# Optimization experiments

Hardware: AMD Instinct MI355X
Metric: run time of the kernel (lower is better)

## Reference

```python
import jax, jax.numpy as jnp
import numpy as np

B, N, F_IN, H, C, K = 32, 1024, 128, 64, 32, 2
L_HOP, NUM_ITER, TEMP = 2, 5, 0.5


def setup_inputs() -> dict:
    key = jax.random.key(0)
    ks = jax.random.split(key, 8)
    x = jax.random.normal(ks[0], (B, N, F_IN), jnp.float32)
    adj = jax.random.randint(ks[1], (B, N, N), 0, 2, jnp.int32)  # dense 0/1 adjacency per graph
    W_gcn = jax.random.normal(ks[2], (F_IN, H), jnp.float32) / np.sqrt(F_IN)
    b_gcn = jnp.zeros((H,), jnp.float32)
    W_unary = jax.random.normal(ks[3], (H, C), jnp.float32) / np.sqrt(H)
    b_unary = jnp.zeros((C,), jnp.float32)
    means = jax.random.normal(ks[4], (K, H), jnp.float32)
    scales = jnp.ones((K, H), jnp.float32) * 8.0  # widened so exp(-dist) stays in fp32 range
    kw = jnp.ones((K,), jnp.float32)
    mu = jax.random.normal(ks[5], (C, C), jnp.float32)
    return dict(x=x, adj=adj, W_gcn=W_gcn, b_gcn=b_gcn, W_unary=W_unary,
                b_unary=b_unary, means=means, scales=scales, kw=kw, mu=mu)


def _forward(x, adj_f, W_gcn, b_gcn, W_unary, b_unary, means, scales, kw, mu):
    n = x.shape[1]
    # --- GCN encode: D^{-1/2}(A+I)D^{-1/2} X W + b, relu ---
    a_hat = adj_f + jnp.eye(n, dtype=adj_f.dtype)
    dinv = jax.lax.rsqrt(a_hat.sum(-1))                       # [B,N], deg >= 1 via self-loop
    norm = dinv[:, :, None] * a_hat * dinv[:, None, :]        # [B,N,N]
    h = jax.nn.relu(jnp.einsum('bij,bjf,fh->bih', norm, x, W_gcn) + b_gcn)  # [B,N,H]
    # --- l-hop reachability mask ---
    adj_l = adj_f
    for _ in range(L_HOP - 1):
        adj_l = adj_l @ adj_f
    adj_l = (adj_l > 0).astype(h.dtype)                       # [B,N,N]
    # --- unary potentials ---
    unary = h @ W_unary + b_unary                             # [B,N,C]
    # --- Gaussian kernel: w_k * exp(dist_i[k] + dist_j[k]) == (e*w) @ e.T ---
    diff = (h[:, :, None, :] - means) / scales                # [B,N,K,H]
    e = jnp.exp(-jnp.sum(diff * diff, -1))                    # [B,N,K]
    pairwise = jnp.einsum('bik,k,bjk->bij', e, kw, e) * adj_l  # [B,N,N]
    # --- mean-field CRF iterations ---
    Q = jax.nn.softmax(unary, -1)
    for _ in range(NUM_ITER):
        msg = jnp.einsum('bij,bjc->bic', pairwise, Q @ mu)
        Q = jax.nn.softmax((unary + msg) / TEMP, -1)
    # --- soft-cluster pooling ---
    x_pooled = jnp.einsum('bnc,bnh->bch', Q, h)               # [B,C,H]
    adj_pooled = jnp.einsum('bnc,bnm,bmd->bcd', Q, adj_f, Q)  # [B,C,C]
    return x_pooled, adj_pooled


def reference(x, adj, W_gcn, b_gcn, W_unary, b_unary, means, scales, kw, mu):
    return _forward(x, adj.astype(x.dtype), W_gcn, b_gcn, W_unary, b_unary,
                    means, scales, kw, mu)
```

## Files before the change

### kernel.cpp

```cpp
#include <hip/hip_runtime.h>
#include <stdint.h>

#define NB  32
#define NN  1024
#define FIN 128
#define HH  64
#define CC  32
#define ZCAP 16
#define NITER 5

using short8  = __attribute__((ext_vector_type(8))) short;
using floatx4 = __attribute__((ext_vector_type(4))) float;

__device__ inline float b2f(unsigned short u) {
  union { uint32_t i; float f; } v; v.i = ((uint32_t)u) << 16; return v.f;
}
__device__ inline float b2f_lo(uint32_t w) {
  union { uint32_t i; float f; } v; v.i = w << 16; return v.f;
}
__device__ inline float b2f_hi(uint32_t w) {
  union { uint32_t i; float f; } v; v.i = w & 0xFFFF0000u; return v.f;
}
__device__ inline unsigned short f2b(float f) {
  union { uint32_t i; float f; } v; v.f = f;
  uint32_t r = v.i + 0x7FFFu + ((v.i >> 16) & 1u);
  return (unsigned short)(r >> 16);
}
__device__ inline floatx4 zf4() { floatx4 v = {0.f, 0.f, 0.f, 0.f}; return v; }

__global__ __launch_bounds__(256) void k_wcvt(const float* __restrict__ Wg,
    const float* __restrict__ Wu, unsigned short* __restrict__ Wgt,
    unsigned short* __restrict__ Wut, float* __restrict__ out, int out_n) {
  const int t = threadIdx.x;
  for (int idx = t; idx < HH * FIN; idx += 256) {
    int hh = idx >> 7, f = idx & 127;
    Wgt[idx] = f2b(Wg[f * HH + hh]);
  }
  for (int idx = t; idx < CC * HH; idx += 256) {
    int c = idx >> 6, f = idx & 63;
    Wut[idx] = f2b(Wu[f * CC + c]);
  }
  for (int idx = t; idx < out_n; idx += 256) out[idx] = 0.f;
}

__global__ __launch_bounds__(256) void k_bits(const int* __restrict__ adj,
    uint32_t* __restrict__ rowbits, float* __restrict__ dinv,
    int* __restrict__ zcnt) {
  __shared__ uint32_t rw[4][32];
  const int t = threadIdx.x, g = t >> 6, lane = t & 63;
  if (lane < 32) rw[g][lane] = 0u;
  __syncthreads();
  const size_t row = (size_t)blockIdx.x * 4 + g;
  int s = 0;
  #pragma unroll
  for (int rep = 0; rep < 4; rep++) {
    int4 a = ((const int4*)(adj + row * NN))[rep * 64 + lane];
    int b0 = (a.x != 0), b1 = (a.y != 0), b2 = (a.z != 0), b3 = (a.w != 0);
    uint32_t nib = ((uint32_t)(b0 | (b1 << 1) | (b2 << 2) | (b3 << 3))) << ((lane & 7) * 4);
    atomicOr(&rw[g][rep * 8 + (lane >> 3)], nib);
    s += b0 + b1 + b2 + b3;
  }
  #pragma unroll
  for (int m = 1; m < 64; m <<= 1) s += __shfl_xor(s, m, 64);
  __syncthreads();
  if (lane < 32) rowbits[row * 32 + lane] = rw[g][lane];
  if (lane == 0) { dinv[row] = rsqrtf((float)s + 1.0f); zcnt[row] = 0; }
}

__global__ __launch_bounds__(256) void k_cbits(const uint32_t* __restrict__ rowbits,
    uint32_t* __restrict__ colbits) {
  __shared__ uint32_t rbL[512 * 32];
  const int bid = blockIdx.x;
  const int b = bid >> 3, half = (bid >> 2) & 1, jt = bid & 3;
  const int t = threadIdx.x;
  const uint32_t* src = rowbits + ((size_t)b * NN + half * 512) * 32;
  for (int idx = t; idx < 512 * 32; idx += 256) rbL[idx] = src[idx];
  __syncthreads();
  const int j = jt * 256 + t, jw = j >> 5, jb = j & 31;
  uint32_t out[16];
  for (int w = 0; w < 16; w++) {
    uint32_t acc = 0;
    #pragma unroll
    for (int r = 0; r < 32; r++)
      acc |= ((rbL[(w * 32 + r) * 32 + jw] >> jb) & 1u) << r;
    out[w] = acc;
  }
  uint4* dst = (uint4*)(colbits + ((size_t)b * NN + j) * 32 + half * 16);
  #pragma unroll
  for (int x = 0; x < 4; x++) {
    uint4 v; v.x = out[4*x]; v.y = out[4*x+1]; v.z = out[4*x+2]; v.w = out[4*x+3];
    dst[x] = v;
  }
}

__global__ __launch_bounds__(256) void k_xw(const float* __restrict__ x,
    const unsigned short* __restrict__ Wgt, const float* __restrict__ dinv,
    unsigned short* __restrict__ xs, unsigned short* __restrict__ xst) {
  const int bid = blockIdx.x;
  const int b = bid >> 4;
  const int m0 = (bid & 15) * 64;
  const int t = threadIdx.x, wv = t >> 6, lane = t & 63, l15 = lane & 15, q = lane >> 4;
  const int mb = m0 + wv * 16;
  floatx4 acc[4];
  #pragma unroll
  for (int u = 0; u < 4; u++) acc[u] = zf4();
  #pragma unroll
  for (int k0 = 0; k0 < FIN; k0 += 32) {
    const float4* xp = (const float4*)(x + ((size_t)b * NN + mb + l15) * FIN + k0 + q * 8);
    float4 a0 = xp[0], a1 = xp[1];
    short8 af;
    af[0] = (short)f2b(a0.x); af[1] = (short)f2b(a0.y);
    af[2] = (short)f2b(a0.z); af[3] = (short)f2b(a0.w);
    af[4] = (short)f2b(a1.x); af[5] = (short)f2b(a1.y);
    af[6] = (short)f2b(a1.z); af[7] = (short)f2b(a1.w);
    #pragma unroll
    for (int u = 0; u < 4; u++) {
      short8 bf = *(const short8*)(Wgt + (u * 16 + l15) * FIN + k0 + q * 8);
      acc[u] = __builtin_amdgcn_mfma_f32_16x16x32_bf16(af, bf, acc[u], 0, 0, 0);
    }
  }
  #pragma unroll
  for (int r = 0; r < 4; r++) {
    const int i = mb + q * 4 + r;
    const float dv = dinv[b * NN + i];
    #pragma unroll
    for (int u = 0; u < 4; u++) {
      const int c = u * 16 + l15;
      unsigned short bv = f2b(dv * acc[u][r]);
      xs[((size_t)b * NN + i) * HH + c] = bv;
      xst[((size_t)b * HH + c) * NN + i] = bv;
    }
  }
}

__global__ __launch_bounds__(256) void k_gcnun(const uint32_t* __restrict__ rowbits,
    const unsigned short* __restrict__ xst, const unsigned short* __restrict__ xs,
    const float* __restrict__ dinv, const float* __restrict__ bg,
    const float* __restrict__ means, const float* __restrict__ scales,
    const unsigned short* __restrict__ Wut, const float* __restrict__ bu,
    float* __restrict__ h, float* __restrict__ e2, float* __restrict__ unary) {
  __shared__ unsigned short hsh[4][16][72];
  const int bid = blockIdx.x;
  const int b = bid >> 4;
  const int m0 = (bid & 15) * 64;
  const int t = threadIdx.x, wv = t >> 6, lane = t & 63, l15 = lane & 15, q = lane >> 4;
  const int mb = m0 + wv * 16;
  floatx4 acc[4];
  #pragma unroll
  for (int u = 0; u < 4; u++) acc[u] = zf4();
  const uint32_t* rbrow = rowbits + ((size_t)b * NN + mb + l15) * 32;
  for (int k0 = 0; k0 < NN; k0 += 32) {
    uint32_t sh = rbrow[k0 >> 5] >> (q * 8);
    short8 af;
    #pragma unroll
    for (int jj = 0; jj < 8; jj++)
      af[jj] = (short)(((sh >> jj) & 1u) ? 0x3F80 : 0);
    #pragma unroll
    for (int u = 0; u < 4; u++) {
      short8 bf = *(const short8*)(xst + ((size_t)b * HH + u * 16 + l15) * NN + k0 + q * 8);
      acc[u] = __builtin_amdgcn_mfma_f32_16x16x32_bf16(af, bf, acc[u], 0, 0, 0);
    }
  }
  float bgc[4], mn0[4], mn1[4], is0[4], is1[4];
  #pragma unroll
  for (int u = 0; u < 4; u++) {
    const int c = u * 16 + l15;
    bgc[u] = bg[c];
    mn0[u] = means[c];        is0[u] = 1.0f / scales[c];
    mn1[u] = means[HH + c];   is1[u] = 1.0f / scales[HH + c];
  }
  #pragma unroll
  for (int r = 0; r < 4; r++) {
    const int i = mb + q * 4 + r;
    const float dv = dinv[b * NN + i];
    float dd0 = 0.f, dd1 = 0.f;
    #pragma unroll
    for (int u = 0; u < 4; u++) {
      const int c = u * 16 + l15;
      float xsv = b2f(xs[((size_t)b * NN + i) * HH + c]);
      float v = dv * (acc[u][r] + xsv) + bgc[u];
      v = v > 0.f ? v : 0.f;
      h[((size_t)b * NN + i) * HH + c] = v;
      unsigned short hb = f2b(v);
      hsh[wv][q * 4 + r][c] = hb;
      float vb = b2f(hb);
      float t0 = (vb - mn0[u]) * is0[u]; dd0 += t0 * t0;
      float t1 = (vb - mn1[u]) * is1[u]; dd1 += t1 * t1;
    }
    #pragma unroll
    for (int m = 1; m < 16; m <<= 1) {
      dd0 += __shfl_xor(dd0, m, 64);
      dd1 += __shfl_xor(dd1, m, 64);
    }
    if (l15 == 0) {
      e2[((size_t)b * NN + i) * 2 + 0] = __expf(-dd0);
      e2[((size_t)b * NN + i) * 2 + 1] = __expf(-dd1);
    }
  }
  floatx4 uacc[2];
  uacc[0] = zf4(); uacc[1] = zf4();
  #pragma unroll
  for (int k0 = 0; k0 < HH; k0 += 32) {
    short8 af = *(const short8*)&hsh[wv][l15][k0 + q * 8];
    #pragma unroll
    for (int u = 0; u < 2; u++) {
      short8 bf = *(const short8*)(Wut + (u * 16 + l15) * HH + k0 + q * 8);
      uacc[u] = __builtin_amdgcn_mfma_f32_16x16x32_bf16(af, bf, uacc[u], 0, 0, 0);
    }
  }
  const float bu0 = bu[l15], bu1 = bu[16 + l15];
  #pragma unroll
  for (int r = 0; r < 4; r++) {
    const int i = mb + q * 4 + r;
    unary[((size_t)b * NN + i) * CC + l15] = uacc[0][r] + bu0;
    unary[((size_t)b * NN + i) * CC + 16 + l15] = uacc[1][r] + bu1;
  }
}

__global__ __launch_bounds__(256) void k_zscan(const uint32_t* __restrict__ rowbits,
    const uint32_t* __restrict__ colbits, int* __restrict__ zcnt,
    int* __restrict__ zidx) {
  __shared__ uint32_t rwL[128 * 32];
  const int bid = blockIdx.x;
  const int b = bid >> 3, it = bid & 7;
  const int i0 = it * 128;
  const int t = threadIdx.x;
  #pragma unroll
  for (int x = 0; x < 16; x++)
    rwL[x * 256 + t] = rowbits[((size_t)b * NN + i0) * 32 + x * 256 + t];
  __syncthreads();
  for (int jc = 0; jc < 4; jc++) {
    const int j = jc * 256 + t;
    uint32_t cb[32];
    const uint4* cbp = (const uint4*)(colbits + ((size_t)b * NN + j) * 32);
    #pragma unroll
    for (int x = 0; x < 8; x++) {
      uint4 v = cbp[x];
      cb[4*x] = v.x; cb[4*x+1] = v.y; cb[4*x+2] = v.z; cb[4*x+3] = v.w;
    }
    for (int i = 0; i < 128; i++) {
      uint32_t m = 0;
      for (int w = 0; w < 32; w++) {
        m |= rwL[i * 32 + w] & cb[w];
        if (__all(m != 0)) break;
      }
      if (m == 0) {
        int old = atomicAdd(&zcnt[b * NN + i0 + i], 1);
        if (old < ZCAP) zidx[(size_t)(b * NN + i0 + i) * ZCAP + old] = j;
      }
    }
  }
}

__global__ __launch_bounds__(256) void k_crf1(const float* __restrict__ unary,
    const float* __restrict__ e2g, const float* __restrict__ kwp,
    const float* __restrict__ mu, const uint32_t* __restrict__ rowbits,
    const uint32_t* __restrict__ colbits, const int* __restrict__ zcnt,
    const int* __restrict__ zidx, const float* __restrict__ h,
    unsigned short* __restrict__ qtb, float* __restrict__ out) {
  __shared__ uint32_t QLu[NN * 17];
  __shared__ float eL[NN * 2];
  __shared__ float muL[CC * CC];
  __shared__ float part[4][64];
  __shared__ float Tf[64];
  __shared__ float S[64];
  const int bid = blockIdx.x;
  const int b = bid >> 2, seg = bid & 3;
  const int t = threadIdx.x;
  const float kw0 = kwp[0], kw1 = kwp[1];
  for (int i = t; i < CC * CC; i += 256) muL[i] = mu[i];
  for (int n = t; n < NN; n += 256) {
    float2 ev = ((const float2*)(e2g + ((size_t)b * NN + n) * 2))[0];
    eL[n * 2] = ev.x; eL[n * 2 + 1] = ev.y;
    float lg[CC];
    const float4* ur = (const float4*)(unary + ((size_t)b * NN + n) * CC);
    #pragma unroll
    for (int c4 = 0; c4 < 8; c4++) {
      float4 v = ur[c4];
      lg[c4*4] = v.x; lg[c4*4+1] = v.y; lg[c4*4+2] = v.z; lg[c4*4+3] = v.w;
    }
    float mx = lg[0];
    #pragma unroll
    for (int c = 1; c < CC; c++) mx = fmaxf(mx, lg[c]);
    float s = 0.f;
    #pragma unroll
    for (int c = 0; c < CC; c++) { lg[c] = __expf(lg[c] - mx); s += lg[c]; }
    float inv = 1.f / s;
    #pragma unroll
    for (int d2 = 0; d2 < 16; d2++)
      QLu[n * 17 + d2] = (uint32_t)f2b(lg[2*d2] * inv)
                       | ((uint32_t)f2b(lg[2*d2+1] * inv) << 16);
  }
  __syncthreads();
  const int kd = t & 63, dd = t & 31, kk = (t >> 5) & 1, sub = t >> 6;
  for (int it = 0; it < NITER; it++) {
    float s = 0.f;
    for (int jj = 0; jj < 256; jj++) {
      const int j = sub * 256 + jj;
      const float ej = eL[j * 2 + kk];
      const uint32_t w = QLu[j * 17 + (dd >> 1)];
      s += ej * ((dd & 1) ? b2f_hi(w) : b2f_lo(w));
    }
    part[sub][kd] = s;
    __syncthreads();
    if (t < 64) Tf[t] = part[0][t] + part[1][t] + part[2][t] + part[3][t];
    __syncthreads();
    if (t < 64) {
      const int k = t >> 5, c = t & 31;
      float ss = 0.f;
      #pragma unroll 8
      for (int d = 0; d < CC; d++) ss += Tf[k * 32 + d] * muL[d * 32 + c];
      S[t] = ((k == 0) ? kw0 : kw1) * ss;
    }
    __syncthreads();
    uint32_t newq[4][16];
    #pragma unroll
    for (int rep = 0; rep < 4; rep++) {
      const int n = rep * 256 + t;
      const float e0 = eL[n * 2], e1 = eL[n * 2 + 1];
      float lg[CC];
      {
        const float4* ur = (const float4*)(unary + ((size_t)b * NN + n) * CC);
        const float4* S0 = (const float4*)S;
        const float4* S1 = (const float4*)(S + 32);
        #pragma unroll
        for (int c4 = 0; c4 < 8; c4++) {
          float4 uv = ur[c4], s0 = S0[c4], s1 = S1[c4];
          lg[c4*4]   = uv.x + e0 * s0.x + e1 * s1.x;
          lg[c4*4+1] = uv.y + e0 * s0.y + e1 * s1.y;
          lg[c4*4+2] = uv.z + e0 * s0.z + e1 * s1.z;
          lg[c4*4+3] = uv.w + e0 * s0.w + e1 * s1.w;
        }
      }
      const int zc = zcnt[b * NN + n];
      if (zc > 0) {
        if (zc <= ZCAP) {
          for (int z = 0; z < zc; z++) {
            const int j = zidx[(size_t)(b * NN + n) * ZCAP + z];
            const float w = kw0 * e0 * eL[j * 2] + kw1 * e1 * eL[j * 2 + 1];
            for (int d2 = 0; d2 < 16; d2++) {
              const uint32_t wq = QLu[j * 17 + d2];
              const float w0 = w * b2f_lo(wq), w1 = w * b2f_hi(wq);
              #pragma unroll 8
              for (int c = 0; c < CC; c++)
                lg[c] -= w0 * muL[(2*d2) * 32 + c] + w1 * muL[(2*d2+1) * 32 + c];
            }
          }
        } else {
          const uint32_t* rbi = rowbits + ((size_t)b * NN + n) * 32;
          for (int j = 0; j < NN; j++) {
            uint32_t m = 0;
            const uint32_t* cbj = colbits + ((size_t)b * NN + j) * 32;
            for (int w32 = 0; w32 < 32; w32++) m |= rbi[w32] & cbj[w32];
            if (m == 0) {
              const float w = kw0 * e0 * eL[j * 2] + kw1 * e1 * eL[j * 2 + 1];
              for (int d2 = 0; d2 < 16; d2++) {
                const uint32_t wq = QLu[j * 17 + d2];
                const float w0 = w * b2f_lo(wq), w1 = w * b2f_hi(wq);
                #pragma unroll 8
                for (int c = 0; c < CC; c++)
                  lg[c] -= w0 * muL[(2*d2) * 32 + c] + w1 * muL[(2*d2+1) * 32 + c];
              }
            }
          }
        }
      }
      float mx = lg[0];
      #pragma unroll
      for (int c = 1; c < CC; c++) mx = fmaxf(mx, lg[c]);
      float ss = 0.f;
      #pragma unroll
      for (int c = 0; c < CC; c++) { lg[c] = __expf((lg[c] - mx) * 2.0f); ss += lg[c]; }
      const float inv = 1.f / ss;
      #pragma unroll
      for (int d2 = 0; d2 < 16; d2++)
        newq[rep][d2] = (uint32_t)f2b(lg[2*d2] * inv)
                      | ((uint32_t)f2b(lg[2*d2+1] * inv) << 16);
    }
    __syncthreads();
    #pragma unroll
    for (int rep = 0; rep < 4; rep++) {
      const int n = rep * 256 + t;
      #pragma unroll
      for (int d2 = 0; d2 < 16; d2++) QLu[n * 17 + d2] = newq[rep][d2];
    }
    __syncthreads();
  }
  {
    const int n = seg * 256 + t;
    #pragma unroll
    for (int d2 = 0; d2 < 16; d2++) {
      const uint32_t w = QLu[n * 17 + d2];
      qtb[((size_t)b * CC + 2*d2) * NN + n]     = (unsigned short)(w & 0xFFFFu);
      qtb[((size_t)b * CC + 2*d2 + 1) * NN + n] = (unsigned short)(w >> 16);
    }
  }
  {
    const int hh = t & 63, cg = t >> 6;
    float acc[8] = {0, 0, 0, 0, 0, 0, 0, 0};
    const int j0 = seg * 256;
    for (int jj = 0; jj < 256; jj++) {
      const int j = j0 + jj;
      const float hv = h[((size_t)b * NN + j) * HH + hh];
      #pragma unroll
      for (int w = 0; w < 4; w++) {
        const uint32_t q2 = QLu[j * 17 + cg * 4 + w];
        acc[2*w]     += b2f_lo(q2) * hv;
        acc[2*w + 1] += b2f_hi(q2) * hv;
      }
    }
    #pragma unroll
    for (int k = 0; k < 8; k++)
      atomicAdd(&out[((size_t)b * CC + cg * 8 + k) * HH + hh], acc[k]);
  }
}

__global__ __launch_bounds__(256) void k_adjqp(const uint32_t* __restrict__ rowbits,
    const unsigned short* __restrict__ qtb, float* __restrict__ out) {
  __shared__ float adjL[64][33];
  __shared__ float qL[64][32];
  const int bid = blockIdx.x;
  const int b = bid >> 4;
  const int m0 = (bid & 15) * 64;
  const int t = threadIdx.x, wv = t >> 6, lane = t & 63, l15 = lane & 15, q = lane >> 4;
  const int mb = m0 + wv * 16;
  floatx4 acc[2];
  acc[0] = zf4(); acc[1] = zf4();
  const uint32_t* rbrow = rowbits + ((size_t)b * NN + mb + l15) * 32;
  for (int k0 = 0; k0 < NN; k0 += 32) {
    uint32_t sh = rbrow[k0 >> 5] >> (q * 8);
    short8 af;
    #pragma unroll
    for (int jj = 0; jj < 8; jj++)
      af[jj] = (short)(((sh >> jj) & 1u) ? 0x3F80 : 0);
    #pragma unroll
    for (int u = 0; u < 2; u++) {
      short8 bf = *(const short8*)(qtb + ((size_t)b * CC + u * 16 + l15) * NN + k0 + q * 8);
      acc[u] = __builtin_amdgcn_mfma_f32_16x16x32_bf16(af, bf, acc[u], 0, 0, 0);
    }
  }
  #pragma unroll
  for (int r = 0; r < 4; r++)
    #pragma unroll
    for (int u = 0; u < 2; u++)
      adjL[wv * 16 + q * 4 + r][u * 16 + l15] = acc[u][r];
  #pragma unroll
  for (int x = 0; x < 8; x++) {
    const int idx = x * 256 + t;
    const int i = idx & 63, c = idx >> 6;
    qL[i][c] = b2f(qtb[((size_t)b * CC + c) * NN + m0 + i]);
  }
  __syncthreads();
  const int d = t & 31, cg = t >> 5;
  float a2[4] = {0, 0, 0, 0};
  for (int i = 0; i < 64; i++) {
    const float av = adjL[i][d];
    #pragma unroll
    for (int k = 0; k < 4; k++) a2[k] += qL[i][cg * 4 + k] * av;
  }
  #pragma unroll
  for (int k = 0; k < 4; k++)
    atomicAdd(&out[(size_t)NB * CC * HH + ((size_t)b * CC + cg * 4 + k) * CC + d], a2[k]);
}

extern "C" void kernel_launch(void* const* d_in, const int* in_sizes, int n_in,
                              void* d_out, int out_size, void* d_ws, size_t ws_size,
                              hipStream_t stream) {
  (void)in_sizes; (void)n_in; (void)out_size;
  const float* x      = (const float*)d_in[0];
  const int*   adj    = (const int*)d_in[1];
  const float* Wg     = (const float*)d_in[2];
  const float* bg     = (const float*)d_in[3];
  const float* Wu     = (const float*)d_in[4];
  const float* bu     = (const float*)d_in[5];
  const float* means  = (const float*)d_in[6];
  const float* scales = (const float*)d_in[7];
  const float* kw     = (const float*)d_in[8];
  const float* mu     = (const float*)d_in[9];

  char* ws = (char*)d_ws;
  size_t off = 0;
  auto alloc = [&](size_t bytes) { char* p = ws + off; off += (bytes + 255) & ~(size_t)255; return p; };
  uint32_t*       rbits = (uint32_t*)alloc((size_t)NB * NN * 32 * 4);
  uint32_t*       cbits = (uint32_t*)alloc((size_t)NB * NN * 32 * 4);
  float*          dinv  = (float*)alloc((size_t)NB * NN * 4);
  unsigned short* Wgt   = (unsigned short*)alloc((size_t)HH * FIN * 2);
  unsigned short* Wut   = (unsigned short*)alloc((size_t)CC * HH * 2);
  unsigned short* xs    = (unsigned short*)alloc((size_t)NB * NN * HH * 2);
  unsigned short* xst   = (unsigned short*)alloc((size_t)NB * HH * NN * 2);
  float*          h     = (float*)alloc((size_t)NB * NN * HH * 4);
  float*          e2    = (float*)alloc((size_t)NB * NN * 2 * 4);
  float*          unary = (float*)alloc((size_t)NB * NN * CC * 4);
  int*            zcnt  = (int*)alloc((size_t)NB * NN * 4);
  int*            zidx  = (int*)alloc((size_t)NB * NN * ZCAP * 4);
  unsigned short* qtb   = (unsigned short*)alloc((size_t)NB * CC * NN * 2);
  if (off > ws_size) return;

  float* out = (float*)d_out;
  const int out_n = NB * CC * (HH + CC);

  k_wcvt <<<1, 256, 0, stream>>>(Wg, Wu, Wgt, Wut, out, out_n);
  k_bits <<<NB * NN / 4, 256, 0, stream>>>(adj, rbits, dinv, zcnt);
  k_cbits<<<NB * 8, 256, 0, stream>>>(rbits, cbits);
  k_zscan<<<NB * 8, 256, 0, stream>>>(rbits, cbits, zcnt, zidx);
  k_xw   <<<NB * 16, 256, 0, stream>>>(x, Wgt, dinv, xs, xst);
  k_gcnun<<<NB * 16, 256, 0, stream>>>(rbits, xst, xs, dinv, bg, means, scales,
                                       Wut, bu, h, e2, unary);
  k_crf1 <<<NB * 4, 256, 0, stream>>>(unary, e2, kw, mu, rbits, cbits,
                                      zcnt, zidx, h, qtb, out);
  k_adjqp<<<NB * 16, 256, 0, stream>>>(rbits, qtb, out);
}
```

Measured before the change: 437.8 us.

## Split CRF iterations into per-iteration kernels with global Q ping-pong

```diff
diff --git a/kernel.cpp b/kernel.cpp
--- a/kernel.cpp
+++ b/kernel.cpp
@@ -138,11 +138,14 @@
     const float* __restrict__ dinv, const float* __restrict__ bg,
     const float* __restrict__ means, const float* __restrict__ scales,
     const unsigned short* __restrict__ Wut, const float* __restrict__ bu,
-    float* __restrict__ h, float* __restrict__ e2, float* __restrict__ unary) {
+    float* __restrict__ h, float* __restrict__ e2, float* __restrict__ unary,
+    unsigned short* __restrict__ Q0, float* __restrict__ Tp0) {
   __shared__ unsigned short hsh[4][16][72];
+  __shared__ float Qs0[64][33];
+  __shared__ float es0[64][2];
   const int bid = blockIdx.x;
-  const int b = bid >> 4;
-  const int m0 = (bid & 15) * 64;
+  const int b = bid >> 4, blk = bid & 15;
+  const int m0 = blk * 64;
   const int t = threadIdx.x, wv = t >> 6, lane = t & 63, l15 = lane & 15, q = lane >> 4;
   const int mb = m0 + wv * 16;
   floatx4 acc[4];
@@ -193,8 +196,11 @@
       dd1 += __shfl_xor(dd1, m, 64);
     }
     if (l15 == 0) {
-      e2[((size_t)b * NN + i) * 2 + 0] = __expf(-dd0);
-      e2[((size_t)b * NN + i) * 2 + 1] = __expf(-dd1);
+      float ev0 = __expf(-dd0), ev1 = __expf(-dd1);
+      e2[((size_t)b * NN + i) * 2 + 0] = ev0;
+      e2[((size_t)b * NN + i) * 2 + 1] = ev1;
+      es0[wv * 16 + q * 4 + r][0] = ev0;
+      es0[wv * 16 + q * 4 + r][1] = ev1;
     }
   }
   floatx4 uacc[2];
@@ -212,8 +218,32 @@
   #pragma unroll
   for (int r = 0; r < 4; r++) {
     const int i = mb + q * 4 + r;
-    unary[((size_t)b * NN + i) * CC + l15] = uacc[0][r] + bu0;
-    unary[((size_t)b * NN + i) * CC + 16 + l15] = uacc[1][r] + bu1;
+    const int iloc = wv * 16 + q * 4 + r;
+    float a0 = uacc[0][r] + bu0;
+    float a1 = uacc[1][r] + bu1;
+    unary[((size_t)b * NN + i) * CC + l15] = a0;
+    unary[((size_t)b * NN + i) * CC + 16 + l15] = a1;
+    float mx = fmaxf(a0, a1);
+    #pragma unroll
+    for (int m = 1; m < 16; m <<= 1) mx = fmaxf(mx, __shfl_xor(mx, m, 64));
+    float x0 = __expf(a0 - mx), x1 = __expf(a1 - mx);
+    float s = x0 + x1;
+    #pragma unroll
+    for (int m = 1; m < 16; m <<= 1) s += __shfl_xor(s, m, 64);
+    float inv = 1.f / s;
+    float q0v = x0 * inv, q1v = x1 * inv;
+    Q0[((size_t)b * NN + i) * CC + l15] = f2b(q0v);
+    Q0[((size_t)b * NN + i) * CC + 16 + l15] = f2b(q1v);
+    Qs0[iloc][l15] = q0v;
+    Qs0[iloc][16 + l15] = q1v;
+  }
+  __syncthreads();
+  if (t < 64) {
+    const int k = t >> 5, d = t & 31;
+    float s = 0.f;
+    #pragma unroll 8
+    for (int i = 0; i < 64; i++) s += es0[i][k] * Qs0[i][d];
+    Tp0[((size_t)b * 16 + blk) * 64 + t] = s;
   }
 }
 
@@ -252,166 +282,146 @@
   }
 }
 
-__global__ __launch_bounds__(256) void k_crf1(const float* __restrict__ unary,
-    const float* __restrict__ e2g, const float* __restrict__ kwp,
-    const float* __restrict__ mu, const uint32_t* __restrict__ rowbits,
-    const uint32_t* __restrict__ colbits, const int* __restrict__ zcnt,
-    const int* __restrict__ zidx, const float* __restrict__ h,
-    unsigned short* __restrict__ qtb, float* __restrict__ out) {
-  __shared__ uint32_t QLu[NN * 17];
-  __shared__ float eL[NN * 2];
+__global__ __launch_bounds__(256) void k_supd2(const float* __restrict__ unary,
+    const float* __restrict__ e2g, const float* __restrict__ TpIn, int npart,
+    const float* __restrict__ mu, const float* __restrict__ kwp,
+    const int* __restrict__ zcnt, const int* __restrict__ zidx,
+    const unsigned short* __restrict__ Qprev, unsigned short* __restrict__ Qnext,
+    float* __restrict__ TpOut, const uint32_t* __restrict__ rowbits,
+    const uint32_t* __restrict__ colbits, const float* __restrict__ h,
+    unsigned short* __restrict__ qtb, float* __restrict__ out, int last) {
   __shared__ float muL[CC * CC];
-  __shared__ float part[4][64];
   __shared__ float Tf[64];
   __shared__ float S[64];
+  __shared__ uint32_t qs[256][17];
+  __shared__ float es[256][2];
+  __shared__ float part[4][64];
   const int bid = blockIdx.x;
   const int b = bid >> 2, seg = bid & 3;
   const int t = threadIdx.x;
-  const float kw0 = kwp[0], kw1 = kwp[1];
   for (int i = t; i < CC * CC; i += 256) muL[i] = mu[i];
-  for (int n = t; n < NN; n += 256) {
-    float2 ev = ((const float2*)(e2g + ((size_t)b * NN + n) * 2))[0];
-    eL[n * 2] = ev.x; eL[n * 2 + 1] = ev.y;
-    float lg[CC];
-    const float4* ur = (const float4*)(unary + ((size_t)b * NN + n) * CC);
+  if (t < 64) {
+    float s = 0.f;
+    for (int p = 0; p < npart; p++) s += TpIn[((size_t)b * npart + p) * 64 + t];
+    Tf[t] = s;
+  }
+  __syncthreads();
+  if (t < 64) {
+    const int k = t >> 5, c = t & 31;
+    float ss = 0.f;
+    #pragma unroll 8
+    for (int d = 0; d < CC; d++) ss += Tf[k * 32 + d] * muL[d * 32 + c];
+    S[t] = ((k == 0) ? kwp[0] : kwp[1]) * ss;
+  }
+  __syncthreads();
+  const int n = seg * 256 + t;
+  const int gid = b * NN + n;
+  const float e0 = e2g[(size_t)gid * 2 + 0];
+  const float e1 = e2g[(size_t)gid * 2 + 1];
+  es[t][0] = e0; es[t][1] = e1;
+  float lg[CC];
+  {
+    const float4* ur = (const float4*)(unary + (size_t)gid * CC);
+    const float4* S0 = (const float4*)S;
+    const float4* S1 = (const float4*)(S + 32);
     #pragma unroll
     for (int c4 = 0; c4 < 8; c4++) {
-      float4 v = ur[c4];
-      lg[c4*4] = v.x; lg[c4*4+1] = v.y; lg[c4*4+2] = v.z; lg[c4*4+3] = v.w;
-    }
-    float mx = lg[0];
-    #pragma unroll
-    for (int c = 1; c < CC; c++) mx = fmaxf(mx, lg[c]);
-    float s = 0.f;
-    #pragma unroll
-    for (int c = 0; c < CC; c++) { lg[c] = __expf(lg[c] - mx); s += lg[c]; }
-    float inv = 1.f / s;
-    #pragma unroll
-    for (int d2 = 0; d2 < 16; d2++)
-      QLu[n * 17 + d2] = (uint32_t)f2b(lg[2*d2] * inv)
-                       | ((uint32_t)f2b(lg[2*d2+1] * inv) << 16);
-  }
-  __syncthreads();
-  const int kd = t & 63, dd = t & 31, kk = (t >> 5) & 1, sub = t >> 6;
-  for (int it = 0; it < NITER; it++) {
-    float s = 0.f;
-    for (int jj = 0; jj < 256; jj++) {
-      const int j = sub * 256 + jj;
-      const float ej = eL[j * 2 + kk];
-      const uint32_t w = QLu[j * 17 + (dd >> 1)];
-      s += ej * ((dd & 1) ? b2f_hi(w) : b2f_lo(w));
-    }
-    part[sub][kd] = s;
-    __syncthreads();
-    if (t < 64) Tf[t] = part[0][t] + part[1][t] + part[2][t] + part[3][t];
-    __syncthreads();
-    if (t < 64) {
-      const int k = t >> 5, c = t & 31;
-      float ss = 0.f;
-      #pragma unroll 8
-      for (int d = 0; d < CC; d++) ss += Tf[k * 32 + d] * muL[d * 32 + c];
-      S[t] = ((k == 0) ? kw0 : kw1) * ss;
-    }
-    __syncthreads();
-    uint32_t newq[4][16];
-    #pragma unroll
-    for (int rep = 0; rep < 4; rep++) {
-      const int n = rep * 256 + t;
-      const float e0 = eL[n * 2], e1 = eL[n * 2 + 1];
-      float lg[CC];
-      {
-        const float4* ur = (const float4*)(unary + ((size_t)b * NN + n) * CC);
-        const float4* S0 = (const float4*)S;
-        const float4* S1 = (const float4*)(S + 32);
-        #pragma unroll
-        for (int c4 = 0; c4 < 8; c4++) {
-          float4 uv = ur[c4], s0 = S0[c4], s1 = S1[c4];
-          lg[c4*4]   = uv.x + e0 * s0.x + e1 * s1.x;
-          lg[c4*4+1] = uv.y + e0 * s0.y + e1 * s1.y;
-          lg[c4*4+2] = uv.z + e0 * s0.z + e1 * s1.z;
-          lg[c4*4+3] = uv.w + e0 * s0.w + e1 * s1.w;
+      float4 uv = ur[c4], s0 = S0[c4], s1 = S1[c4];
+      lg[c4*4]   = uv.x + e0 * s0.x + e1 * s1.x;
+      lg[c4*4+1] = uv.y + e0 * s0.y + e1 * s1.y;
+      lg[c4*4+2] = uv.z + e0 * s0.z + e1 * s1.z;
+      lg[c4*4+3] = uv.w + e0 * s0.w + e1 * s1.w;
+    }
+  }
+  const int zc = zcnt[gid];
+  if (zc > 0) {
+    const float kw0 = kwp[0], kw1 = kwp[1];
+    if (zc <= ZCAP) {
+      for (int z = 0; z < zc; z++) {
+        const int j = zidx[(size_t)gid * ZCAP + z];
+        const float w = kw0 * e0 * e2g[((size_t)b * NN + j) * 2 + 0]
+                      + kw1 * e1 * e2g[((size_t)b * NN + j) * 2 + 1];
+        const unsigned short* qj = Qprev + ((size_t)b * NN + j) * CC;
+        for (int d = 0; d < CC; d++) {
+          const float wq = w * b2f(qj[d]);
+          #pragma unroll 8
+          for (int c = 0; c < CC; c++) lg[c] -= wq * muL[d * CC + c];
         }
       }
-      const int zc = zcnt[b * NN + n];
-      if (zc > 0) {
-        if (zc <= ZCAP) {
-          for (int z = 0; z < zc; z++) {
-            const int j = zidx[(size_t)(b * NN + n) * ZCAP + z];
-            const float w = kw0 * e0 * eL[j * 2] + kw1 * e1 * eL[j * 2 + 1];
-            for (int d2 = 0; d2 < 16; d2++) {
-              const uint32_t wq = QLu[j * 17 + d2];
-              const float w0 = w * b2f_lo(wq), w1 = w * b2f_hi(wq);
-              #pragma unroll 8
-              for (int c = 0; c < CC; c++)
-                lg[c] -= w0 * muL[(2*d2) * 32 + c] + w1 * muL[(2*d2+1) * 32 + c];
-            }
-          }
-        } else {
-          const uint32_t* rbi = rowbits + ((size_t)b * NN + n) * 32;
-          for (int j = 0; j < NN; j++) {
-            uint32_t m = 0;
-            const uint32_t* cbj = colbits + ((size_t)b * NN + j) * 32;
-            for (int w32 = 0; w32 < 32; w32++) m |= rbi[w32] & cbj[w32];
-            if (m == 0) {
-              const float w = kw0 * e0 * eL[j * 2] + kw1 * e1 * eL[j * 2 + 1];
-              for (int d2 = 0; d2 < 16; d2++) {
-                const uint32_t wq = QLu[j * 17 + d2];
-                const float w0 = w * b2f_lo(wq), w1 = w * b2f_hi(wq);
-                #pragma unroll 8
-                for (int c = 0; c < CC; c++)
-                  lg[c] -= w0 * muL[(2*d2) * 32 + c] + w1 * muL[(2*d2+1) * 32 + c];
-              }
-            }
+    } else {
+      const uint32_t* rbi = rowbits + (size_t)gid * 32;
+      for (int j = 0; j < NN; j++) {
+        uint32_t m = 0;
+        const uint32_t* cbj = colbits + ((size_t)b * NN + j) * 32;
+        for (int w32 = 0; w32 < 32; w32++) m |= rbi[w32] & cbj[w32];
+        if (m == 0) {
+          const float kw0b = kwp[0], kw1b = kwp[1];
+          const float w = kw0b * e0 * e2g[((size_t)b * NN + j) * 2 + 0]
+                        + kw1b * e1 * e2g[((size_t)b * NN + j) * 2 + 1];
+          const unsigned short* qj = Qprev + ((size_t)b * NN + j) * CC;
+          for (int d = 0; d < CC; d++) {
+            const float wq = w * b2f(qj[d]);
+            #pragma unroll 8
+            for (int c = 0; c < CC; c++) lg[c] -= wq * muL[d * CC + c];
           }
         }
       }
-      float mx = lg[0];
-      #pragma unroll
-      for (int c = 1; c < CC; c++) mx = fmaxf(mx, lg[c]);
-      float ss = 0.f;
-      #pragma unroll
-      for (int c = 0; c < CC; c++) { lg[c] = __expf((lg[c] - mx) * 2.0f); ss += lg[c]; }
-      const float inv = 1.f / ss;
-      #pragma unroll
-      for (int d2 = 0; d2 < 16; d2++)
-        newq[rep][d2] = (uint32_t)f2b(lg[2*d2] * inv)
-                      | ((uint32_t)f2b(lg[2*d2+1] * inv) << 16);
-    }
+    }
+  }
+  float mx = lg[0];
+  #pragma unroll
+  for (int c = 1; c < CC; c++) mx = fmaxf(mx, lg[c]);
+  float ss = 0.f;
+  #pragma unroll
+  for (int c = 0; c < CC; c++) { lg[c] = __expf((lg[c] - mx) * 2.0f); ss += lg[c]; }
+  const float inv = 1.f / ss;
+  uint32_t pk[16];
+  #pragma unroll
+  for (int d2 = 0; d2 < 16; d2++) {
+    pk[d2] = (uint32_t)f2b(lg[2*d2] * inv) | ((uint32_t)f2b(lg[2*d2+1] * inv) << 16);
+    qs[t][d2] = pk[d2];
+  }
+  if (!last) {
+    uint32_t* qn = (uint32_t*)(Qnext + (size_t)gid * CC);
+    #pragma unroll
+    for (int d2 = 0; d2 < 16; d2++) qn[d2] = pk[d2];
+  }
+  __syncthreads();
+  if (!last) {
+    const int kd = t & 63, d = t & 31, k = (t >> 5) & 1, sub = t >> 6;
+    float s = 0.f;
+    #pragma unroll 4
+    for (int jj = 0; jj < 64; jj++) {
+      const int j = sub * 64 + jj;
+      const uint32_t w = qs[j][d >> 1];
+      s += es[j][k] * ((d & 1) ? b2f_hi(w) : b2f_lo(w));
+    }
+    part[sub][kd] = s;
     __syncthreads();
-    #pragma unroll
-    for (int rep = 0; rep < 4; rep++) {
-      const int n = rep * 256 + t;
-      #pragma unroll
-      for (int d2 = 0; d2 < 16; d2++) QLu[n * 17 + d2] = newq[rep][d2];
-    }
-    __syncthreads();
-  }
-  {
-    const int n = seg * 256 + t;
-    #pragma unroll
-    for (int d2 = 0; d2 < 16; d2++) {
-      const uint32_t w = QLu[n * 17 + d2];
-      qtb[((size_t)b * CC + 2*d2) * NN + n]     = (unsigned short)(w & 0xFFFFu);
-      qtb[((size_t)b * CC + 2*d2 + 1) * NN + n] = (unsigned short)(w >> 16);
-    }
-  }
-  {
+    if (t < 64)
+      TpOut[((size_t)b * 4 + seg) * 64 + t] = part[0][t] + part[1][t] + part[2][t] + part[3][t];
+  } else {
+    #pragma unroll
+    for (int c = 0; c < CC; c++) {
+      const uint32_t w = pk[c >> 1];
+      qtb[((size_t)b * CC + c) * NN + n] =
+          (unsigned short)((c & 1) ? (w >> 16) : (w & 0xFFFFu));
+    }
     const int hh = t & 63, cg = t >> 6;
     float acc[8] = {0, 0, 0, 0, 0, 0, 0, 0};
-    const int j0 = seg * 256;
     for (int jj = 0; jj < 256; jj++) {
-      const int j = j0 + jj;
+      const int j = seg * 256 + jj;
       const float hv = h[((size_t)b * NN + j) * HH + hh];
       #pragma unroll
       for (int w = 0; w < 4; w++) {
-        const uint32_t q2 = QLu[j * 17 + cg * 4 + w];
+        const uint32_t q2 = qs[jj][cg * 4 + w];
         acc[2*w]     += b2f_lo(q2) * hv;
         acc[2*w + 1] += b2f_hi(q2) * hv;
       }
     }
     #pragma unroll
-    for (int k = 0; k < 8; k++)
-      atomicAdd(&out[((size_t)b * CC + cg * 8 + k) * HH + hh], acc[k]);
+    for (int k2 = 0; k2 < 8; k2++)
+      atomicAdd(&out[((size_t)b * CC + cg * 8 + k2) * HH + hh], acc[k2]);
   }
 }
 
@@ -493,7 +503,12 @@
   float*          unary = (float*)alloc((size_t)NB * NN * CC * 4);
   int*            zcnt  = (int*)alloc((size_t)NB * NN * 4);
   int*            zidx  = (int*)alloc((size_t)NB * NN * ZCAP * 4);
+  unsigned short* Qa    = (unsigned short*)alloc((size_t)NB * NN * CC * 2);
+  unsigned short* Qb    = (unsigned short*)alloc((size_t)NB * NN * CC * 2);
   unsigned short* qtb   = (unsigned short*)alloc((size_t)NB * CC * NN * 2);
+  float*          Tp0   = (float*)alloc((size_t)NB * 16 * 64 * 4);
+  float*          TpA   = (float*)alloc((size_t)NB * 4 * 64 * 4);
+  float*          TpB   = (float*)alloc((size_t)NB * 4 * 64 * 4);
   if (off > ws_size) return;
 
   float* out = (float*)d_out;
@@ -505,8 +520,17 @@
   k_zscan<<<NB * 8, 256, 0, stream>>>(rbits, cbits, zcnt, zidx);
   k_xw   <<<NB * 16, 256, 0, stream>>>(x, Wgt, dinv, xs, xst);
   k_gcnun<<<NB * 16, 256, 0, stream>>>(rbits, xst, xs, dinv, bg, means, scales,
-                                       Wut, bu, h, e2, unary);
-  k_crf1 <<<NB * 4, 256, 0, stream>>>(unary, e2, kw, mu, rbits, cbits,
-                                      zcnt, zidx, h, qtb, out);
+                                       Wut, bu, h, e2, unary, Qa, Tp0);
+  unsigned short* qprev = Qa; unsigned short* qnext = Qb;
+  const float* tin = Tp0; int npart = 16; float* tout = TpA;
+  for (int it = 0; it < NITER; it++) {
+    const int last = (it == NITER - 1) ? 1 : 0;
+    k_supd2<<<NB * 4, 256, 0, stream>>>(unary, e2, tin, npart, mu, kw, zcnt, zidx,
+                                        qprev, qnext, tout, rbits, cbits, h,
+                                        qtb, out, last);
+    unsigned short* tmpq = qprev; qprev = qnext; qnext = tmpq;
+    tin = tout; npart = 4;
+    tout = (tout == TpA) ? TpB : TpA;
+  }
   k_adjqp<<<NB * 16, 256, 0, stream>>>(rbits, qtb, out);
 }
```

Measured after the change: 419.1 us. 4.3% less time.
